# Kernel tuning notes

Measured on AMD Instinct MI355X. Metric: run time of the kernel, lower is better.

Reference implementation:

```python
import jax, jax.numpy as jnp
import numpy as np

EPS = 1e-5

def _conv(x, w, pad):
    # x: [B,C,H,W] NCHW, w: [O,I,kh,kw] OIHW
    return jax.lax.conv_general_dilated(
        x, w, (1, 1), [(pad, pad), (pad, pad)],
        dimension_numbers=('NCHW', 'OIHW', 'NCHW'))

def _bn(x, g, b, m, v):
    # eval-mode batchnorm folded into scale/shift
    s = g * jax.lax.rsqrt(v + EPS)
    return x * s[None, :, None, None] + (b - m * s)[None, :, None, None]

def _cbr(x, w, g, b, m, v):
    # Convolution block from CornerNet: conv3x3(pad=1, no bias) + BN + ReLU
    return jax.nn.relu(_bn(_conv(x, w, 1), g, b, m, v))


def setup_inputs() -> dict:
    key = jax.random.key(0)
    B, Cin, C, H, W = 4, 256, 256, 128, 128
    kdims = {'up': (C, Cin, 3, 3), 'down': (C, Cin, 3, 3),
             'p': (C, C, 3, 3), 'c1': (C, Cin, 1, 1), 'c2': (C, C, 3, 3)}
    inp = {'x': jax.random.normal(key, (B, Cin, H, W), dtype=jnp.float32)}
    for i, n in enumerate(['up', 'down', 'p', 'c1', 'c2']):
        ks = jax.random.split(jax.random.fold_in(key, i + 1), 5)
        inp['w_' + n] = jax.random.normal(ks[0], kdims[n], dtype=jnp.float32) * 0.02
        inp['g_' + n] = 1.0 + 0.1 * jax.random.normal(ks[1], (C,), dtype=jnp.float32)
        inp['b_' + n] = 0.1 * jax.random.normal(ks[2], (C,), dtype=jnp.float32)
        inp['m_' + n] = 0.1 * jax.random.normal(ks[3], (C,), dtype=jnp.float32)
        inp['v_' + n] = 0.5 + jax.random.uniform(ks[4], (C,), dtype=jnp.float32)
    return inp


def reference(x,
              w_up, g_up, b_up, m_up, v_up,
              w_down, g_down, b_down, m_down, v_down,
              w_p, g_p, b_p, m_p, v_p,
              w_c1, g_c1, b_c1, m_c1, v_c1,
              w_c2, g_c2, b_c2, m_c2, v_c2):
    # up branch: conv-bn-relu then LeftPool (reverse cummax over W) then RightPool (cummax over W)
    up = _cbr(x, w_up, g_up, b_up, m_up, v_up)
    up = jax.lax.cummax(up, axis=3, reverse=True)   # LeftPool
    up = jax.lax.cummax(up, axis=3)                 # RightPool
    # down branch: conv-bn-relu then TopPool (reverse cummax over H) then BottomPool (cummax over H)
    down = _cbr(x, w_down, g_down, b_down, m_down, v_down)
    down = jax.lax.cummax(down, axis=2, reverse=True)  # TopPool
    down = jax.lax.cummax(down, axis=2)                # BottomPool
    # merge path: 3x3 conv + BN on pooled sum
    merge = _bn(_conv(up + down, w_p, 1), g_p, b_p, m_p, v_p)
    # shortcut path: 1x1 conv + BN on input
    bn1 = _bn(_conv(x, w_c1, 0), g_c1, b_c1, m_c1, v_c1)
    relu1 = jax.nn.relu(merge + bn1)
    # output Convolution block
    return _cbr(relu1, w_c2, g_c2, b_c2, m_c2, v_c2)
```

## Files before the change

### kernel.cpp

```cpp
#include <hip/hip_runtime.h>

typedef unsigned short u16;
typedef __attribute__((ext_vector_type(8))) short bf16x8;
typedef __attribute__((ext_vector_type(4))) float f32x4;


__device__ __forceinline__ u16 f2bf(float f) {
  unsigned u = __float_as_uint(f);
  unsigned r = u + 0x7fffu + ((u >> 16) & 1u);
  return (u16)(r >> 16);
}

__device__ __forceinline__ void gll16(const char* g, char* l) {
  __builtin_amdgcn_global_load_lds((const __attribute__((address_space(1))) void*)g,
                                   (__attribute__((address_space(3))) void*)l, 16, 0, 0);
}

__global__ void bn_prep_kernel(const float* __restrict__ g, const float* __restrict__ b,
                               const float* __restrict__ m, const float* __restrict__ v,
                               float* __restrict__ st) {
  int c = threadIdx.x;
  float s = g[c] * rsqrtf(v[c] + 1e-5f);
  st[c] = s;
  st[256 + c] = b[c] - m[c] * s;
}

__global__ void bn_fix_kernel(float* __restrict__ st) {
  int c = threadIdx.x;
  st[2 * 512 + 256 + c] += st[3 * 512 + 256 + c];
  st[3 * 512 + c] = st[3 * 512 + c] / st[2 * 512 + c];
}

__global__ void wprep3_kernel(const float* __restrict__ w, u16* __restrict__ dst) {
  int idx = blockIdx.x * 256 + threadIdx.x;
  int e = idx & 7, lane = (idx >> 3) & 63, f = (idx >> 9) & 3, coq = (idx >> 11) & 1;
  int blk = idx >> 12;
  int cohalf = blk / 72, step = blk % 72;
  int outer = step / 12, rr = step % 12, dwi = rr >> 2, kc = rr & 3;
  int half = outer / 3, d = outer % 3;
  int s = d * 3 + dwi;
  int co = cohalf * 128 + coq * 64 + f * 16 + (lane & 15);
  int ci = half * 128 + kc * 32 + (lane >> 4) * 8 + e;
  dst[idx] = f2bf(w[(co * 256 + ci) * 9 + s]);
}

__global__ void wprep1_kernel(const float* __restrict__ w, u16* __restrict__ dst,
                              const float* __restrict__ ratio) {
  int idx = blockIdx.x * 256 + threadIdx.x;
  int e = idx & 7, lane = (idx >> 3) & 63, f = (idx >> 9) & 3, coq = (idx >> 11) & 1;
  int blk = idx >> 12;
  int cohalf = blk >> 3, step = blk & 7;
  int half2 = step >> 2, kc = step & 3;
  int co = cohalf * 128 + coq * 64 + f * 16 + (lane & 15);
  int ci = half2 * 128 + kc * 32 + (lane >> 4) * 8 + e;
  dst[idx] = f2bf(w[co * 256 + ci] * ratio[co]);
}

__global__ __launch_bounds__(256) void nchw_to_nhwc_kernel(const float* __restrict__ x,
                                                           char* __restrict__ xb) {
  __shared__ __align__(16) u16 tl[128 * 130];
  int bh = blockIdx.x; int b = bh >> 7, h = bh & 127;
  int t = threadIdx.x;
  for (int half = 0; half < 2; ++half) {
    __syncthreads();
    for (int i = 0; i < 64; ++i) {
      int cil = i * 2 + (t >> 7);
      int ci = half * 128 + cil;
      int w = t & 127;
      tl[w * 130 + cil] = f2bf(x[(size_t)((b * 256 + ci) * 128 + h) * 128 + w]);
    }
    __syncthreads();
    char* plane = xb + (size_t)(b * 128 + h) * 65536 + half * 32768;
    for (int i = 0; i < 32; ++i) {
      int w = i * 4 + (t >> 6);
      int c2 = (t & 63) * 2;
      unsigned v = *(const unsigned*)&tl[w * 130 + c2];
      *(unsigned*)(plane + w * 256 + ((c2 * 2) ^ (((w + 1) & 7) << 4))) = v;
    }
  }
}

__device__ __forceinline__ void stage_b(const char* plane, char* ldsB, int t) {
  if (plane) {
    char* dst = ldsB + 256 + t * 16;
    const char* g = plane + t * 16;
#pragma unroll
    for (int r = 0; r < 8; ++r) gll16(g + r * 4096, dst + r * 4096);
  } else {
    int4 z = {0, 0, 0, 0};
#pragma unroll
    for (int r = 0; r < 8; ++r) *(int4*)(ldsB + 256 + r * 4096 + t * 16) = z;
  }
}

__device__ __forceinline__ const char* a_ptr(const char* wA1, const char* wA2, int step, int off) {
  const char* src = (step < 72) ? (wA1 + (size_t)step * 8192)
                                : (wA2 + (size_t)(step - 72) * 8192);
  return src + off;
}

__device__ __forceinline__ void zero_acc(f32x4 (&acc)[4][4]) {
  f32x4 z = {0.f, 0.f, 0.f, 0.f};
#pragma unroll
  for (int i = 0; i < 4; ++i)
#pragma unroll
    for (int j = 0; j < 4; ++j) acc[i][j] = z;
}

__device__ __forceinline__ void conv_pipeline(const char* inB1, const char* inB2,
                                              const char* wA1, const char* wA2,
                                              int h, int nsteps, char* lds,
                                              f32x4 (&acc)[4][4]) {
  const int t = threadIdx.x;
  const int wv = t >> 6, lane = t & 63;
  const int lane15 = lane & 15, q = lane >> 4;
  const int coq = wv >> 1, wh = wv & 1;
  char* ldsB = lds;
  const int aoff = coq * 4096 + lane * 16;

  int wpb[4];
#pragma unroll
  for (int f = 0; f < 4; ++f) wpb[f] = wh * 64 + f * 16 + lane15;

  {
    int4 z = {0, 0, 0, 0};
    if (t < 16) *(int4*)(ldsB + t * 16) = z;
    else if (t < 32) *(int4*)(ldsB + 33024 + (t - 16) * 16) = z;
  }

  bf16x8 aB[3][4];
  {
    const char* p0 = a_ptr(wA1, wA2, 0, aoff);
    const char* p1 = a_ptr(wA1, wA2, 1, aoff);
#pragma unroll
    for (int f = 0; f < 4; ++f) aB[0][f] = *(const bf16x8*)(p0 + f * 1024);
#pragma unroll
    for (int f = 0; f < 4; ++f) aB[1][f] = *(const bf16x8*)(p1 + f * 1024);
  }

  for (int outer = 0; outer < 6; ++outer) {
    const int half = (outer >= 3) ? 1 : 0;
    const int d = outer - half * 3;
    const int hs = h + d - 1;
    const char* plane = (hs >= 0 && hs < 128)
                            ? inB1 + (size_t)hs * 65536 + (size_t)half * 32768
                            : nullptr;
    __syncthreads();
    stage_b(plane, ldsB, t);
    __syncthreads();
#pragma unroll
    for (int j = 0; j < 12; ++j) {
      const int dwi = j >> 2, kc = j & 3;
      const int cb = j % 3, pf = (j + 2) % 3;
      int sg = outer * 12 + j + 2;
      if (sg >= nsteps) sg = nsteps - 1;
      const char* p = a_ptr(wA1, wA2, sg, aoff);
#pragma unroll
      for (int f = 0; f < 4; ++f) aB[pf][f] = *(const bf16x8*)(p + f * 1024);
      bf16x8 bf[4];
#pragma unroll
      for (int f = 0; f < 4; ++f) {
        int wp = wpb[f] + dwi;
        bf[f] = *(const bf16x8*)(ldsB + wp * 256 + ((kc * 64 + q * 16) ^ ((wp & 7) << 4)));
      }
      __builtin_amdgcn_s_setprio(1);
#pragma unroll
      for (int fm = 0; fm < 4; ++fm)
#pragma unroll
        for (int fn = 0; fn < 4; ++fn)
          acc[fm][fn] = __builtin_amdgcn_mfma_f32_16x16x32_bf16(aB[cb][fm], bf[fn], acc[fm][fn], 0, 0, 0);
      __builtin_amdgcn_s_setprio(0);
    }
  }
  if (nsteps > 72) {
#pragma unroll
    for (int half2 = 0; half2 < 2; ++half2) {
      __syncthreads();
      stage_b(inB2 + (size_t)h * 65536 + (size_t)half2 * 32768, ldsB, t);
      __syncthreads();
#pragma unroll
      for (int j2 = 0; j2 < 4; ++j2) {
        const int jg = half2 * 4 + j2;
        const int cb = jg % 3, pf = (jg + 2) % 3;
        int sg = 72 + jg + 2;
        if (sg >= nsteps) sg = nsteps - 1;
        const char* p = a_ptr(wA1, wA2, sg, aoff);
#pragma unroll
        for (int f = 0; f < 4; ++f) aB[pf][f] = *(const bf16x8*)(p + f * 1024);
        bf16x8 bf[4];
#pragma unroll
        for (int f = 0; f < 4; ++f) {
          int wp = wpb[f] + 1;
          bf[f] = *(const bf16x8*)(ldsB + wp * 256 + ((j2 * 64 + q * 16) ^ ((wp & 7) << 4)));
        }
        __builtin_amdgcn_s_setprio(1);
#pragma unroll
        for (int fm = 0; fm < 4; ++fm)
#pragma unroll
          for (int fn = 0; fn < 4; ++fn)
            acc[fm][fn] = __builtin_amdgcn_mfma_f32_16x16x32_bf16(aB[cb][fm], bf[fn], acc[fm][fn], 0, 0, 0);
        __builtin_amdgcn_s_setprio(0);
      }
    }
  }
}

__device__ __forceinline__ void store_pad_relu(f32x4 (&acc)[4][4], const float* __restrict__ st,
                                               int cohalf, int b, int h, char* __restrict__ out) {
  const int t = threadIdx.x, lane = t & 63, wv = t >> 6;
  const int lane15 = lane & 15, q = lane >> 4, coq = wv >> 1, wh = wv & 1;
  char* plane = out + (size_t)(b * 128 + h) * 65536 + cohalf * 32768;
#pragma unroll
  for (int fm = 0; fm < 4; ++fm) {
    int co_l = coq * 64 + fm * 16 + q * 4;
    int co = cohalf * 128 + co_l;
    float ss[4], tt[4];
#pragma unroll
    for (int r = 0; r < 4; ++r) { ss[r] = st[co + r]; tt[r] = st[256 + co + r]; }
#pragma unroll
    for (int fn = 0; fn < 4; ++fn) {
      int w = wh * 64 + fn * 16 + lane15;
      short4 o;
      o.x = (short)f2bf(fmaxf(acc[fm][fn][0] * ss[0] + tt[0], 0.f));
      o.y = (short)f2bf(fmaxf(acc[fm][fn][1] * ss[1] + tt[1], 0.f));
      o.z = (short)f2bf(fmaxf(acc[fm][fn][2] * ss[2] + tt[2], 0.f));
      o.w = (short)f2bf(fmaxf(acc[fm][fn][3] * ss[3] + tt[3], 0.f));
      *(short4*)(plane + w * 256 + ((co_l * 2) ^ (((w + 1) & 7) << 4))) = o;
    }
  }
}

__global__ __launch_bounds__(256, 3) void conv_up_kernel(const char* __restrict__ xb,
                                                         const char* __restrict__ wp,
                                                         const float* __restrict__ st,
                                                         float* __restrict__ rmax) {
  __shared__ __align__(16) char lds[33280];
  int swz = (blockIdx.x & 7) * 64 + (blockIdx.x >> 3);
  int b = swz >> 7, h = swz & 127;
  int cohalf = blockIdx.y;
  const char* wA = wp + (size_t)cohalf * 589824;
  f32x4 acc[4][4];
  zero_acc(acc);
  conv_pipeline(xb + (size_t)b * 8388608, nullptr, wA, wA, h, 72, lds, acc);

  const int t = threadIdx.x, lane = t & 63, wv = t >> 6;
  const int lane15 = lane & 15, q = lane >> 4, coq = wv >> 1, wh = wv & 1;
  float* rlds = (float*)lds;
  __syncthreads();
#pragma unroll
  for (int fm = 0; fm < 4; ++fm) {
    int co_l = coq * 64 + fm * 16 + q * 4;
    int co = cohalf * 128 + co_l;
#pragma unroll
    for (int r = 0; r < 4; ++r) {
      float ss = st[co + r], tt = st[256 + co + r];
      float v = 0.f;
#pragma unroll
      for (int fn = 0; fn < 4; ++fn) v = fmaxf(v, acc[fm][fn][r] * ss + tt);
      v = fmaxf(v, __shfl_xor(v, 1));
      v = fmaxf(v, __shfl_xor(v, 2));
      v = fmaxf(v, __shfl_xor(v, 4));
      v = fmaxf(v, __shfl_xor(v, 8));
      if (lane15 == 0) rlds[wh * 128 + co_l + r] = v;
    }
  }
  __syncthreads();
  if (t < 128)
    rmax[(size_t)(b * 128 + h) * 256 + cohalf * 128 + t] = fmaxf(rlds[t], rlds[128 + t]);
}

__global__ __launch_bounds__(256, 3) void conv_down_kernel(const char* __restrict__ xb,
                                                           const char* __restrict__ wp,
                                                           const float* __restrict__ st,
                                                           char* __restrict__ out) {
  __shared__ __align__(16) char lds[33280];
  int swz = (blockIdx.x & 7) * 64 + (blockIdx.x >> 3);
  int b = swz >> 7, h = swz & 127;
  int cohalf = blockIdx.y;
  const char* wA = wp + (size_t)cohalf * 589824;
  f32x4 acc[4][4];
  zero_acc(acc);
  conv_pipeline(xb + (size_t)b * 8388608, nullptr, wA, wA, h, 72, lds, acc);
  store_pad_relu(acc, st, cohalf, b, h, out);
}

__global__ __launch_bounds__(256) void colmax_kernel(const char* __restrict__ dp,
                                                     float* __restrict__ cmax) {
  int bw = blockIdx.x; int b = bw >> 7, w = bw & 127;
  int c = threadIdx.x;
  size_t base = (size_t)b * 8388608 + (size_t)(c >> 7) * 32768 + w * 256 +
                (((c & 127) * 2) ^ (((w + 1) & 7) << 4));
  float m = 0.f;
  for (int h = 0; h < 128; ++h) {
    u16 raw = *(const u16*)(dp + base + (size_t)h * 65536);
    m = fmaxf(m, __uint_as_float(((unsigned)raw) << 16));
  }
  cmax[(size_t)(b * 128 + w) * 256 + c] = m;
}

__global__ __launch_bounds__(256) void pooled_kernel(const float* __restrict__ rmax,
                                                     const float* __restrict__ cmax,
                                                     char* __restrict__ dp) {
  int bh = blockIdx.x; int b = bh >> 7, h = bh & 127;
  int t = threadIdx.x;
  char* plane = dp + (size_t)(b * 128 + h) * 65536;
  const float* rm = rmax + (size_t)(b * 128 + h) * 256;
#pragma unroll
  for (int it = 0; it < 16; ++it) {
    int id = it * 256 + t;
    int half = id >> 11, rem = id & 2047;
    int w = rem >> 4, slot = rem & 15;
    int c0 = half * 128 + slot * 8;
    const float* cm = cmax + (size_t)(b * 128 + w) * 256 + c0;
    const float* rr = rm + c0;
    u16 e[8];
#pragma unroll
    for (int k = 0; k < 8; ++k) e[k] = f2bf(rr[k] + cm[k]);
    int4 v;
    v.x = (int)(e[0] | ((unsigned)e[1] << 16));
    v.y = (int)(e[2] | ((unsigned)e[3] << 16));
    v.z = (int)(e[4] | ((unsigned)e[5] << 16));
    v.w = (int)(e[6] | ((unsigned)e[7] << 16));
    *(int4*)(plane + half * 32768 + w * 256 + ((slot ^ ((w + 1) & 7)) << 4)) = v;
  }
}

__global__ __launch_bounds__(256, 3) void conv_merge_kernel(const char* __restrict__ dp,
                                                            const char* __restrict__ xb,
                                                            const char* __restrict__ wp_p,
                                                            const char* __restrict__ wp_c1,
                                                            const float* __restrict__ st,
                                                            char* __restrict__ out) {
  __shared__ __align__(16) char lds[33280];
  int swz = (blockIdx.x & 7) * 64 + (blockIdx.x >> 3);
  int b = swz >> 7, h = swz & 127;
  int cohalf = blockIdx.y;
  f32x4 acc[4][4];
  zero_acc(acc);
  conv_pipeline(dp + (size_t)b * 8388608, xb + (size_t)b * 8388608,
                wp_p + (size_t)cohalf * 589824, wp_c1 + (size_t)cohalf * 65536,
                h, 80, lds, acc);
  store_pad_relu(acc, st, cohalf, b, h, out);
}

__global__ __launch_bounds__(256, 3) void conv_c2_kernel(const char* __restrict__ relu1,
                                                         const char* __restrict__ wp,
                                                         const float* __restrict__ st,
                                                         float* __restrict__ out) {
  __shared__ __align__(16) char lds[33280];
  int swz = (blockIdx.x & 7) * 64 + (blockIdx.x >> 3);
  int b = swz >> 7, h = swz & 127;
  int cohalf = blockIdx.y;
  const char* wA = wp + (size_t)cohalf * 589824;
  f32x4 acc[4][4];
  zero_acc(acc);
  conv_pipeline(relu1 + (size_t)b * 8388608, nullptr, wA, wA, h, 72, lds, acc);

  const int t = threadIdx.x, lane = t & 63, wv = t >> 6;
  const int lane15 = lane & 15, q = lane >> 4, coq = wv >> 1, wh = wv & 1;
  float* tl = (float*)lds;
  for (int g = 0; g < 8; ++g) {
    __syncthreads();
    if (coq == (g >> 2)) {
      int fm = g & 3;
      int co_l = coq * 64 + fm * 16 + q * 4;
      int co = cohalf * 128 + co_l;
#pragma unroll
      for (int r = 0; r < 4; ++r) {
        float ss = st[co + r], tt = st[256 + co + r];
#pragma unroll
        for (int fn = 0; fn < 4; ++fn) {
          int w = wh * 64 + fn * 16 + lane15;
          tl[(q * 4 + r) * 132 + w] = fmaxf(acc[fm][fn][r] * ss + tt, 0.f);
        }
      }
    }
    __syncthreads();
    int row = t >> 4, ch = t & 15;
    int co = cohalf * 128 + g * 16 + row;
    float* dst = out + (size_t)((b * 256 + co) * 128 + h) * 128 + ch * 8;
    float4 p0 = *(float4*)&tl[row * 132 + ch * 8];
    float4 p1 = *(float4*)&tl[row * 132 + ch * 8 + 4];
    *(float4*)dst = p0;
    *(float4*)(dst + 4) = p1;
  }
}

extern "C" void kernel_launch(void* const* d_in, const int* in_sizes, int n_in,
                              void* d_out, int out_size, void* d_ws, size_t ws_size,
                              hipStream_t stream) {
  (void)in_sizes; (void)n_in; (void)out_size; (void)ws_size;
  const float* x    = (const float*)d_in[0];
  const float* w_up = (const float*)d_in[1];
  const float* w_dn = (const float*)d_in[6];
  const float* w_p  = (const float*)d_in[11];
  const float* w_c1 = (const float*)d_in[16];
  const float* w_c2 = (const float*)d_in[21];

  char* ws = (char*)d_ws;
  char* xb    = ws;
  char* dp    = ws + 33554432ull;
  char* relu1 = ws + 67108864ull;
  char* wp_up = ws + 100663296ull;
  char* wp_dn = ws + 101842944ull;
  char* wp_p  = ws + 103022592ull;
  char* wp_c2 = ws + 104202240ull;
  char* wp_c1 = ws + 105381888ull;
  float* st   = (float*)(ws + 105512960ull);
  float* rmax = (float*)(ws + 105523200ull);
  float* cmax = (float*)(ws + 106047488ull);

  bn_prep_kernel<<<1, 256, 0, stream>>>((const float*)d_in[2], (const float*)d_in[3],
                                        (const float*)d_in[4], (const float*)d_in[5], st);
  bn_prep_kernel<<<1, 256, 0, stream>>>((const float*)d_in[7], (const float*)d_in[8],
                                        (const float*)d_in[9], (const float*)d_in[10], st + 512);
  bn_prep_kernel<<<1, 256, 0, stream>>>((const float*)d_in[12], (const float*)d_in[13],
                                        (const float*)d_in[14], (const float*)d_in[15], st + 1024);
  bn_prep_kernel<<<1, 256, 0, stream>>>((const float*)d_in[17], (const float*)d_in[18],
                                        (const float*)d_in[19], (const float*)d_in[20], st + 1536);
  bn_prep_kernel<<<1, 256, 0, stream>>>((const float*)d_in[22], (const float*)d_in[23],
                                        (const float*)d_in[24], (const float*)d_in[25], st + 2048);
  bn_fix_kernel<<<1, 256, 0, stream>>>(st);

  wprep3_kernel<<<2304, 256, 0, stream>>>(w_up, (u16*)wp_up);
  wprep3_kernel<<<2304, 256, 0, stream>>>(w_dn, (u16*)wp_dn);
  wprep3_kernel<<<2304, 256, 0, stream>>>(w_p, (u16*)wp_p);
  wprep3_kernel<<<2304, 256, 0, stream>>>(w_c2, (u16*)wp_c2);
  wprep1_kernel<<<256, 256, 0, stream>>>(w_c1, (u16*)wp_c1, st + 1536);

  nchw_to_nhwc_kernel<<<512, 256, 0, stream>>>(x, xb);

  conv_up_kernel<<<dim3(512, 2), 256, 0, stream>>>(xb, wp_up, st, rmax);
  conv_down_kernel<<<dim3(512, 2), 256, 0, stream>>>(xb, wp_dn, st + 512, dp);
  colmax_kernel<<<512, 256, 0, stream>>>(dp, cmax);
  pooled_kernel<<<512, 256, 0, stream>>>(rmax, cmax, dp);
  conv_merge_kernel<<<dim3(512, 2), 256, 0, stream>>>(dp, xb, wp_p, wp_c1, st + 1024, relu1);
  conv_c2_kernel<<<dim3(512, 2), 256, 0, stream>>>(relu1, wp_c2, st + 2048, (float*)d_out);
}
```

Baseline: 445.2 us.

## Stage weight tiles through double-buffered LDS with async global-to-LDS loads

Weights are no longer loaded straight from global memory into registers with a three-deep register prefetch. They are now staged into a double-buffered LDS region with global_load_lds, and each k-step waits with explicit waitcnt and a barrier. Weight prep now writes a swizzled per-row layout that matches the new LDS reads, and every conv kernel's LDS grows to about 49KB. The aim is to cut VGPR pressure and global load latency on the A operand. In exchange it adds two barriers per step, and the larger LDS footprint may limit occupancy below the 3 blocks per CU requested in launch bounds.

```diff
diff --git a/kernel.cpp b/kernel.cpp
--- a/kernel.cpp
+++ b/kernel.cpp
@@ -33,26 +33,28 @@
 
 __global__ void wprep3_kernel(const float* __restrict__ w, u16* __restrict__ dst) {
   int idx = blockIdx.x * 256 + threadIdx.x;
-  int e = idx & 7, lane = (idx >> 3) & 63, f = (idx >> 9) & 3, coq = (idx >> 11) & 1;
-  int blk = idx >> 12;
+  int blk = idx >> 12, iu = idx & 4095;
+  int co_l = iu >> 5, w32 = iu & 31, slot = w32 >> 3, e = w32 & 7;
+  int q = slot ^ ((co_l >> 1) & 3);
   int cohalf = blk / 72, step = blk % 72;
   int outer = step / 12, rr = step % 12, dwi = rr >> 2, kc = rr & 3;
   int half = outer / 3, d = outer % 3;
   int s = d * 3 + dwi;
-  int co = cohalf * 128 + coq * 64 + f * 16 + (lane & 15);
-  int ci = half * 128 + kc * 32 + (lane >> 4) * 8 + e;
+  int ci = half * 128 + kc * 32 + q * 8 + e;
+  int co = cohalf * 128 + co_l;
   dst[idx] = f2bf(w[(co * 256 + ci) * 9 + s]);
 }
 
 __global__ void wprep1_kernel(const float* __restrict__ w, u16* __restrict__ dst,
                               const float* __restrict__ ratio) {
   int idx = blockIdx.x * 256 + threadIdx.x;
-  int e = idx & 7, lane = (idx >> 3) & 63, f = (idx >> 9) & 3, coq = (idx >> 11) & 1;
-  int blk = idx >> 12;
-  int cohalf = blk >> 3, step = blk & 7;
-  int half2 = step >> 2, kc = step & 3;
-  int co = cohalf * 128 + coq * 64 + f * 16 + (lane & 15);
-  int ci = half2 * 128 + kc * 32 + (lane >> 4) * 8 + e;
+  int blk = idx >> 12, iu = idx & 4095;
+  int co_l = iu >> 5, w32 = iu & 31, slot = w32 >> 3, e = w32 & 7;
+  int q = slot ^ ((co_l >> 1) & 3);
+  int cohalf = blk >> 3, j = blk & 7;
+  int half2 = j >> 2, kc = j & 3;
+  int ci = half2 * 128 + kc * 32 + q * 8 + e;
+  int co = cohalf * 128 + co_l;
   dst[idx] = f2bf(w[co * 256 + ci] * ratio[co]);
 }
 
@@ -80,6 +82,16 @@
   }
 }
 
+__device__ __forceinline__ void stage_a(const char* wA1, const char* wA2, int step,
+                                        char* ldsA0, int buf, int t) {
+  const char* src = (step < 72) ? (wA1 + (size_t)step * 8192)
+                                : (wA2 + (size_t)(step - 72) * 8192);
+  char* dst = ldsA0 + buf * 8192 + t * 16;
+  const char* g = src + t * 16;
+  gll16(g, dst);
+  gll16(g + 4096, dst + 4096);
+}
+
 __device__ __forceinline__ void stage_b(const char* plane, char* ldsB, int t) {
   if (plane) {
     char* dst = ldsB + 256 + t * 16;
@@ -93,12 +105,6 @@
   }
 }
 
-__device__ __forceinline__ const char* a_ptr(const char* wA1, const char* wA2, int step, int off) {
-  const char* src = (step < 72) ? (wA1 + (size_t)step * 8192)
-                                : (wA2 + (size_t)(step - 72) * 8192);
-  return src + off;
-}
-
 __device__ __forceinline__ void zero_acc(f32x4 (&acc)[4][4]) {
   f32x4 z = {0.f, 0.f, 0.f, 0.f};
 #pragma unroll
@@ -106,6 +112,38 @@
 #pragma unroll
     for (int j = 0; j < 4; ++j) acc[i][j] = z;
 }
+
+#define CONV_STEP(WP_ADD, KC)                                                              \
+  {                                                                                        \
+    if (i + 1 < nsteps) {                                                                  \
+      stage_a(wA1, wA2, i + 1, ldsA0, cur ^ 1, t);                                         \
+      asm volatile("s_waitcnt vmcnt(2) lgkmcnt(0)" ::: "memory");                          \
+    } else {                                                                               \
+      asm volatile("s_waitcnt vmcnt(0) lgkmcnt(0)" ::: "memory");                          \
+    }                                                                                      \
+    __builtin_amdgcn_s_barrier();                                                          \
+    __builtin_amdgcn_sched_barrier(0);                                                     \
+    bf16x8 af[4], bf[4];                                                                   \
+    const char* lA = ldsA0 + cur * 8192;                                                   \
+    _Pragma("unroll")                                                                      \
+    for (int f = 0; f < 4; ++f) af[f] = *(const bf16x8*)(lA + aOff[f]);                    \
+    _Pragma("unroll")                                                                      \
+    for (int f = 0; f < 4; ++f) {                                                          \
+      int wp = wpb[f] + (WP_ADD);                                                          \
+      bf[f] = *(const bf16x8*)(ldsB + wp * 256 + (((KC)*64 + q * 16) ^ ((wp & 7) << 4)));  \
+    }                                                                                      \
+    __builtin_amdgcn_s_setprio(1);                                                         \
+    _Pragma("unroll")                                                                      \
+    for (int fm = 0; fm < 4; ++fm)                                                         \
+      _Pragma("unroll")                                                                    \
+      for (int fn = 0; fn < 4; ++fn)                                                       \
+        acc[fm][fn] =                                                                      \
+            __builtin_amdgcn_mfma_f32_16x16x32_bf16(af[fm], bf[fn], acc[fm][fn], 0, 0, 0); \
+    __builtin_amdgcn_s_setprio(0);                                                         \
+    __builtin_amdgcn_s_barrier();                                                          \
+    cur ^= 1;                                                                              \
+    ++i;                                                                                   \
+  }
 
 __device__ __forceinline__ void conv_pipeline(const char* inB1, const char* inB2,
                                               const char* wA1, const char* wA2,
@@ -116,8 +154,14 @@
   const int lane15 = lane & 15, q = lane >> 4;
   const int coq = wv >> 1, wh = wv & 1;
   char* ldsB = lds;
-  const int aoff = coq * 4096 + lane * 16;
-
+  char* ldsA0 = lds + 33280;
+
+  int aOff[4];
+#pragma unroll
+  for (int f = 0; f < 4; ++f) {
+    int ra = coq * 64 + f * 16 + lane15;
+    aOff[f] = ra * 64 + ((q ^ ((ra >> 1) & 3)) << 4);
+  }
   int wpb[4];
 #pragma unroll
   for (int f = 0; f < 4; ++f) wpb[f] = wh * 64 + f * 16 + lane15;
@@ -128,16 +172,7 @@
     else if (t < 32) *(int4*)(ldsB + 33024 + (t - 16) * 16) = z;
   }
 
-  bf16x8 aB[3][4];
-  {
-    const char* p0 = a_ptr(wA1, wA2, 0, aoff);
-    const char* p1 = a_ptr(wA1, wA2, 1, aoff);
-#pragma unroll
-    for (int f = 0; f < 4; ++f) aB[0][f] = *(const bf16x8*)(p0 + f * 1024);
-#pragma unroll
-    for (int f = 0; f < 4; ++f) aB[1][f] = *(const bf16x8*)(p1 + f * 1024);
-  }
-
+  int cur = 0, i = 0;
   for (int outer = 0; outer < 6; ++outer) {
     const int half = (outer >= 3) ? 1 : 0;
     const int d = outer - half * 3;
@@ -145,62 +180,18 @@
     const char* plane = (hs >= 0 && hs < 128)
                             ? inB1 + (size_t)hs * 65536 + (size_t)half * 32768
                             : nullptr;
-    __syncthreads();
     stage_b(plane, ldsB, t);
-    __syncthreads();
-#pragma unroll
-    for (int j = 0; j < 12; ++j) {
-      const int dwi = j >> 2, kc = j & 3;
-      const int cb = j % 3, pf = (j + 2) % 3;
-      int sg = outer * 12 + j + 2;
-      if (sg >= nsteps) sg = nsteps - 1;
-      const char* p = a_ptr(wA1, wA2, sg, aoff);
-#pragma unroll
-      for (int f = 0; f < 4; ++f) aB[pf][f] = *(const bf16x8*)(p + f * 1024);
-      bf16x8 bf[4];
-#pragma unroll
-      for (int f = 0; f < 4; ++f) {
-        int wp = wpb[f] + dwi;
-        bf[f] = *(const bf16x8*)(ldsB + wp * 256 + ((kc * 64 + q * 16) ^ ((wp & 7) << 4)));
-      }
-      __builtin_amdgcn_s_setprio(1);
-#pragma unroll
-      for (int fm = 0; fm < 4; ++fm)
-#pragma unroll
-        for (int fn = 0; fn < 4; ++fn)
-          acc[fm][fn] = __builtin_amdgcn_mfma_f32_16x16x32_bf16(aB[cb][fm], bf[fn], acc[fm][fn], 0, 0, 0);
-      __builtin_amdgcn_s_setprio(0);
-    }
+    if (outer == 0) stage_a(wA1, wA2, 0, ldsA0, 0, t);
+#pragma unroll
+    for (int dwi = 0; dwi < 3; ++dwi)
+#pragma unroll
+      for (int kc = 0; kc < 4; ++kc) CONV_STEP(dwi, kc)
   }
   if (nsteps > 72) {
-#pragma unroll
     for (int half2 = 0; half2 < 2; ++half2) {
-      __syncthreads();
       stage_b(inB2 + (size_t)h * 65536 + (size_t)half2 * 32768, ldsB, t);
-      __syncthreads();
-#pragma unroll
-      for (int j2 = 0; j2 < 4; ++j2) {
-        const int jg = half2 * 4 + j2;
-        const int cb = jg % 3, pf = (jg + 2) % 3;
-        int sg = 72 + jg + 2;
-        if (sg >= nsteps) sg = nsteps - 1;
-        const char* p = a_ptr(wA1, wA2, sg, aoff);
-#pragma unroll
-        for (int f = 0; f < 4; ++f) aB[pf][f] = *(const bf16x8*)(p + f * 1024);
-        bf16x8 bf[4];
-#pragma unroll
-        for (int f = 0; f < 4; ++f) {
-          int wp = wpb[f] + 1;
-          bf[f] = *(const bf16x8*)(ldsB + wp * 256 + ((j2 * 64 + q * 16) ^ ((wp & 7) << 4)));
-        }
-        __builtin_amdgcn_s_setprio(1);
-#pragma unroll
-        for (int fm = 0; fm < 4; ++fm)
-#pragma unroll
-          for (int fn = 0; fn < 4; ++fn)
-            acc[fm][fn] = __builtin_amdgcn_mfma_f32_16x16x32_bf16(aB[cb][fm], bf[fn], acc[fm][fn], 0, 0, 0);
-        __builtin_amdgcn_s_setprio(0);
-      }
+#pragma unroll
+      for (int kc = 0; kc < 4; ++kc) CONV_STEP(1, kc)
     }
   }
 }
@@ -234,7 +225,7 @@
                                                          const char* __restrict__ wp,
                                                          const float* __restrict__ st,
                                                          float* __restrict__ rmax) {
-  __shared__ __align__(16) char lds[33280];
+  __shared__ __align__(16) char lds[49664];
   int swz = (blockIdx.x & 7) * 64 + (blockIdx.x >> 3);
   int b = swz >> 7, h = swz & 127;
   int cohalf = blockIdx.y;
@@ -273,7 +264,7 @@
                                                            const char* __restrict__ wp,
                                                            const float* __restrict__ st,
                                                            char* __restrict__ out) {
-  __shared__ __align__(16) char lds[33280];
+  __shared__ __align__(16) char lds[49664];
   int swz = (blockIdx.x & 7) * 64 + (blockIdx.x >> 3);
   int b = swz >> 7, h = swz & 127;
   int cohalf = blockIdx.y;
@@ -331,7 +322,7 @@
                                                             const char* __restrict__ wp_c1,
                                                             const float* __restrict__ st,
                                                             char* __restrict__ out) {
-  __shared__ __align__(16) char lds[33280];
+  __shared__ __align__(16) char lds[49664];
   int swz = (blockIdx.x & 7) * 64 + (blockIdx.x >> 3);
   int b = swz >> 7, h = swz & 127;
   int cohalf = blockIdx.y;
@@ -347,7 +338,7 @@
                                                          const char* __restrict__ wp,
                                                          const float* __restrict__ st,
                                                          float* __restrict__ out) {
-  __shared__ __align__(16) char lds[33280];
+  __shared__ __align__(16) char lds[49664];
   int swz = (blockIdx.x & 7) * 64 + (blockIdx.x >> 3);
   int b = swz >> 7, h = swz & 127;
   int cohalf = blockIdx.y;
```

Measured after the change: 399.5 us. -10.3%, faster.
